# Optimization experiments

Hardware: AMD Instinct MI355X
Metric: run time of the kernel (lower is better)

The kernel has to match this reference:

```python
import jax, jax.numpy as jnp
import numpy as np

DIM = 768
NUM_HEADS = 12
HEAD_DIM = DIM // NUM_HEADS
SCALE = HEAD_DIM ** -0.5


def setup_inputs() -> dict:
    key = jax.random.key(0)
    ks = jax.random.split(key, 6)
    B, Lq, Lkv = 8, 1024, 1024
    return {
        "q": jax.random.normal(ks[0], (B, Lq, DIM), dtype=jnp.float32),
        "kv": jax.random.normal(ks[1], (B, Lkv, DIM), dtype=jnp.float32),
        "attn_pos": jax.random.normal(ks[2], (1, NUM_HEADS, Lq, Lkv), dtype=jnp.float32),
        "Wq": jax.random.normal(ks[3], (DIM, DIM), dtype=jnp.float32) * (DIM ** -0.5),
        "Wkv": jax.random.normal(ks[4], (2 * DIM, DIM), dtype=jnp.float32) * (DIM ** -0.5),
        "Wproj": jax.random.normal(ks[5], (DIM, DIM), dtype=jnp.float32) * (DIM ** -0.5),
        "bproj": jnp.zeros((DIM,), dtype=jnp.float32),
    }


def reference(q, kv, attn_pos, Wq, Wkv, Wproj, bproj):
    B, Lq, C = q.shape
    Lkv = kv.shape[1]
    H, D = NUM_HEADS, HEAD_DIM
    # q/kv projections (torch Linear: x @ W.T); attn_pos_encoding_only path
    qh = (q @ Wq.T).reshape(B, Lq, H, D).transpose(0, 2, 1, 3)        # (B,H,Lq,D)
    kvp = (kv @ Wkv.T).reshape(B, Lkv, 2, H, D).transpose(2, 0, 3, 1, 4)
    k, v = kvp[0], kvp[1]                                             # (B,H,Lkv,D)
    # scaled dot-product attention with additive positional bias
    attn = jnp.einsum('bhqd,bhkd->bhqk', qh, k) * SCALE + attn_pos    # (B,H,Lq,Lkv)
    attn = jax.nn.softmax(attn, axis=-1)
    x = jnp.einsum('bhqk,bhkd->bhqd', attn, v)                        # (B,H,Lq,D)
    x = x.transpose(0, 2, 1, 3).reshape(B, Lq, C)
    return x @ Wproj.T + bproj
```

## Files before the change

kernel.cpp:

```cpp
#include <hip/hip_runtime.h>

#define DIM 768
#define NHEADS 12
#define HDIM 64
#define BATCH 8
#define LQ 1024
#define LKV 1024
#define ATTN_SCALE 0.125f
#define LOG2E 1.4426950408889634f
#define C1_SL2E 0.18033688011112042f

typedef __bf16 bf16;
typedef __bf16 bf16x4 __attribute__((ext_vector_type(4)));
typedef __bf16 bf16x8 __attribute__((ext_vector_type(8)));
typedef short s16x4 __attribute__((ext_vector_type(4)));
typedef float f32x4 __attribute__((ext_vector_type(4)));

union B4 { bf16x4 h; s16x4 s; };

static __device__ __forceinline__ f32x4 mfma_k32(bf16x8 a, bf16x8 b, f32x4 c) {
    return __builtin_amdgcn_mfma_f32_16x16x32_bf16(a, b, c, 0, 0, 0);
}
static __device__ __forceinline__ f32x4 mfma_k16(s16x4 a, s16x4 b, f32x4 c) {
    return __builtin_amdgcn_mfma_f32_16x16x16bf16_1k(a, b, c, 0, 0, 0);
}

static __device__ __forceinline__ void async16(const bf16* g, bf16* l) {
    __builtin_amdgcn_global_load_lds(
        (const __attribute__((address_space(1))) unsigned int*)g,
        (__attribute__((address_space(3))) unsigned int*)l, 16, 0, 0);
}
static __device__ __forceinline__ void drain_vmem() {
    __asm__ volatile("s_waitcnt vmcnt(0)" ::: "memory");
}
#define WAIT_VMCNT(N) __asm__ volatile("s_waitcnt vmcnt(" #N ")" ::: "memory")
static __device__ __forceinline__ void code_fence() {
    __asm__ volatile("" ::: "memory");
}

#define NQ4 (BATCH * LQ * DIM / 4)
#define NW4 (DIM * DIM / 4)
__global__ void cvt_all(const float4* __restrict__ q, const float4* __restrict__ kv,
                        const float4* __restrict__ Wq, const float4* __restrict__ Wkv,
                        const float4* __restrict__ Wp,
                        bf16x4* __restrict__ qb, bf16x4* __restrict__ kvb,
                        bf16x4* __restrict__ wall, bf16x4* __restrict__ wpb) {
    int i = blockIdx.x * 256 + threadIdx.x;
    const float4* src; bf16x4* dst; int j;
    if (i < NQ4)                { src = q;   dst = qb;        j = i; }
    else if (i < 2 * NQ4)       { src = kv;  dst = kvb;       j = i - NQ4; }
    else if (i < 2 * NQ4 + NW4) { src = Wq;  dst = wall;      j = i - 2 * NQ4; }
    else if (i < 2 * NQ4 + 3 * NW4) { src = Wkv; dst = wall + NW4; j = i - 2 * NQ4 - NW4; }
    else if (i < 2 * NQ4 + 4 * NW4) { src = Wp;  dst = wpb;   j = i - 2 * NQ4 - 3 * NW4; }
    else return;
    float4 v = src[j];
    bf16x4 o;
    o[0] = (bf16)v.x; o[1] = (bf16)v.y; o[2] = (bf16)v.z; o[3] = (bf16)v.w;
    dst[j] = o;
}

__global__ __launch_bounds__(256) void proj_gemm(
    const bf16* __restrict__ qb, const bf16* __restrict__ kvb,
    const bf16* __restrict__ W,
    bf16* __restrict__ Qp, bf16* __restrict__ Kp, bf16* __restrict__ Vt)
{
    __shared__ bf16 As[2][128 * 32];
    __shared__ bf16 Bs[2][128 * 32];
    const int tid  = threadIdx.x;
    const int lane = tid & 63;
    const int w    = tid >> 6;
    const int wm = (w >> 1) * 64;
    const int wn = (w & 1) * 64;
    const int m0 = blockIdx.x * 128;
    const int n0 = blockIdx.y * 128;
    const int K = DIM;
    const int lq = lane & 15;
    const int quad = lane >> 4;

    const bf16* A = (n0 < DIM) ? qb : kvb;
    const int isV = (n0 >= 2 * DIM);

    const int rl = lane >> 2;
    const int ck = (lane & 3) * 8;
    const bf16* gA = A + (size_t)(m0 + w * 32 + rl) * K + ck;
    const bf16* gB = W + (size_t)(n0 + w * 32 + rl) * K + ck;

    f32x4 acc[4][4] = {};

#define PSTAGE(K0, BUFI) do {                                          \
    async16(gA + (K0),                  &As[BUFI][w * 1024]);          \
    async16(gA + (size_t)16 * K + (K0), &As[BUFI][w * 1024 + 512]);    \
    async16(gB + (K0),                  &Bs[BUFI][w * 1024]);          \
    async16(gB + (size_t)16 * K + (K0), &Bs[BUFI][w * 1024 + 512]);    \
} while (0)

    PSTAGE(0, 0);
    drain_vmem();
    __syncthreads();

    for (int k0 = 0; k0 < K; k0 += 32) {
        const int cur = (k0 >> 5) & 1;
        const bool more = (k0 + 32 < K);
        if (more) PSTAGE(k0 + 32, cur ^ 1);

        bf16x8 a[4], b[4];
        #pragma unroll
        for (int i = 0; i < 4; i++)
            a[i] = *(const bf16x8*)&As[cur][(wm + i * 16 + lq) * 32 + quad * 8];
        #pragma unroll
        for (int j = 0; j < 4; j++)
            b[j] = *(const bf16x8*)&Bs[cur][(wn + j * 16 + lq) * 32 + quad * 8];
        if (isV) {
            #pragma unroll
            for (int i = 0; i < 4; i++)
                #pragma unroll
                for (int j = 0; j < 4; j++)
                    acc[i][j] = mfma_k32(a[i], b[j], acc[i][j]);
        } else {
            #pragma unroll
            for (int i = 0; i < 4; i++)
                #pragma unroll
                for (int j = 0; j < 4; j++)
                    acc[i][j] = mfma_k32(b[j], a[i], acc[i][j]);
        }

        if (more) drain_vmem();
        __syncthreads();
    }
#undef PSTAGE

    if (isV) {
        const int n0v = n0 - 2 * DIM;
        #pragma unroll
        for (int i = 0; i < 4; i++) {
            const int base_m = m0 + wm + i * 16;
            const int b_idx = base_m >> 10;
            const int kvl = (base_m & 1023) + quad * 4;
            #pragma unroll
            for (int j = 0; j < 4; j++) {
                const int nl = n0v + wn + j * 16 + lq;
                const int h = nl >> 6;
                const int d = nl & 63;
                B4 pk;
                #pragma unroll
                for (int r = 0; r < 4; r++) pk.h[r] = (bf16)acc[i][j][r];
                *(s16x4*)&Vt[(((size_t)b_idx * NHEADS + h) * HDIM + d) * LKV + kvl] = pk.s;
            }
        }
    } else {
        bf16* Cb = (n0 < DIM) ? Qp : Kp;
        const float cs = (n0 < DIM) ? C1_SL2E : 1.0f;
        const int nb = (n0 < DIM) ? n0 : n0 - DIM;
        #pragma unroll
        for (int i = 0; i < 4; i++) {
            const size_t row = m0 + wm + i * 16 + lq;
            #pragma unroll
            for (int j = 0; j < 4; j++) {
                const int col = nb + wn + j * 16 + quad * 4;
                B4 pk;
                #pragma unroll
                for (int r = 0; r < 4; r++) pk.h[r] = (bf16)(acc[i][j][r] * cs);
                *(s16x4*)&Cb[row * DIM + col] = pk.s;
            }
        }
    }
}

__global__ __launch_bounds__(256) void out_gemm(
    const bf16* __restrict__ A, const bf16* __restrict__ B,
    float* __restrict__ Cp, const float* __restrict__ bias, int M, int N, int K)
{
    __shared__ bf16 As[2][64 * 32];
    __shared__ bf16 Bs[2][128 * 32];
    const int tid  = threadIdx.x;
    const int lane = tid & 63;
    const int w    = tid >> 6;
    const int wm = (w >> 1) * 32;
    const int wn = (w & 1) * 64;
    const int m0 = blockIdx.x * 64;
    const int n0 = blockIdx.y * 128;
    const int lq = lane & 15;
    const int quad = lane >> 4;

    const int rl = lane >> 2;
    const int ck = (lane & 3) * 8;
    const bf16* gA = A + (size_t)(m0 + w * 16 + rl) * K + ck;
    const bf16* gB = B + (size_t)(n0 + w * 32 + rl) * K + ck;

    f32x4 acc[2][4] = {};

#define OSTAGE(K0, BUFI) do {                                          \
    async16(gA + (K0),                  &As[BUFI][w * 512]);           \
    async16(gB + (K0),                  &Bs[BUFI][w * 1024]);          \
    async16(gB + (size_t)16 * K + (K0), &Bs[BUFI][w * 1024 + 512]);    \
} while (0)

    OSTAGE(0, 0);
    drain_vmem();
    __syncthreads();

    for (int k0 = 0; k0 < K; k0 += 32) {
        const int cur = (k0 >> 5) & 1;
        const bool more = (k0 + 32 < K);
        if (more) OSTAGE(k0 + 32, cur ^ 1);

        bf16x8 a[2], b[4];
        #pragma unroll
        for (int i = 0; i < 2; i++)
            a[i] = *(const bf16x8*)&As[cur][(wm + i * 16 + lq) * 32 + quad * 8];
        #pragma unroll
        for (int j = 0; j < 4; j++)
            b[j] = *(const bf16x8*)&Bs[cur][(wn + j * 16 + lq) * 32 + quad * 8];
        #pragma unroll
        for (int i = 0; i < 2; i++)
            #pragma unroll
            for (int j = 0; j < 4; j++)
                acc[i][j] = mfma_k32(b[j], a[i], acc[i][j]);

        if (more) drain_vmem();
        __syncthreads();
    }
#undef OSTAGE

    #pragma unroll
    for (int i = 0; i < 2; i++) {
        const size_t row = m0 + wm + i * 16 + lq;
        #pragma unroll
        for (int j = 0; j < 4; j++) {
            const int col = n0 + wn + j * 16 + quad * 4;
            float4 bj = *(const float4*)&bias[col];
            float4 o;
            o.x = acc[i][j][0] + bj.x; o.y = acc[i][j][1] + bj.y;
            o.z = acc[i][j][2] + bj.z; o.w = acc[i][j][3] + bj.w;
            *(float4*)&Cp[row * N + col] = o;
        }
    }
}

__global__ __launch_bounds__(256) void attn_kernel(
    const bf16* __restrict__ Qb,
    const bf16* __restrict__ Kb,
    const bf16* __restrict__ Vt,
    const float* __restrict__ pos,
    bf16* __restrict__ O)
{
    __shared__ bf16 Ks[2][64 * 64];
    __shared__ bf16 Vs[2][64 * 64];

    const int by = blockIdx.y;
    const int h = by >> 3, b = by & 7;
    const int bh = b * NHEADS + h;
    const int q0 = blockIdx.x * 64;
    const int t = threadIdx.x;
    const int lane = t & 63;
    const int w = t >> 6;
    const int lq = lane & 15;
    const int quad = lane >> 4;

    const bf16* qg = Qb + (size_t)(b * LQ + q0 + w * 16 + lq) * DIM + h * HDIM + quad * 8;
    bf16x8 qa0 = *(const bf16x8*)(qg);
    bf16x8 qa1 = *(const bf16x8*)(qg + 32);

    const int srow  = t >> 3;
    const int chunk = t & 7;
    const int sw    = (chunk ^ (srow & 7)) * 8;
    const bf16* Kg = Kb + (size_t)(b * LKV + srow) * DIM + h * HDIM + sw;
    const bf16* Vg = Vt + (size_t)(bh * HDIM + srow) * LKV + sw;

#define STAGE(kv0, bufi) do {                                                                 \
    async16(Kg + (size_t)(kv0) * DIM,        &Ks[bufi][srow * 64 + chunk * 8]);               \
    async16(Kg + (size_t)((kv0) + 32) * DIM, &Ks[bufi][(srow + 32) * 64 + chunk * 8]);        \
    async16(Vg + (kv0),                      &Vs[bufi][srow * 64 + chunk * 8]);               \
    async16(Vg + (size_t)32 * LKV + (kv0),   &Vs[bufi][(srow + 32) * 64 + chunk * 8]);        \
} while (0)

#define NT (LKV / 64)

    const float4* pos4 = (const float4*)(pos + ((size_t)h * LQ + q0 + w * 16 + lq) * LKV);

    float l_r = 0.f;
    f32x4 o_acc[4] = {};

    STAGE(0, 0);
    float4 pA0 = pos4[quad],      pA1 = pos4[4 + quad];
    float4 pA2 = pos4[8 + quad],  pA3 = pos4[12 + quad];
    float4 pB0 = pos4[16 + quad], pB1 = pos4[20 + quad];
    float4 pB2 = pos4[24 + quad], pB3 = pos4[28 + quad];
    WAIT_VMCNT(8);
    __builtin_amdgcn_s_barrier();
    code_fence();

#define SMB(KB, P) do {                                          \
    float p0 = exp2f(fmaf((P).x, LOG2E, sc[KB][0]));             \
    float p1 = exp2f(fmaf((P).y, LOG2E, sc[KB][1]));             \
    float p2 = exp2f(fmaf((P).z, LOG2E, sc[KB][2]));             \
    float p3 = exp2f(fmaf((P).w, LOG2E, sc[KB][3]));             \
    l_r += (p0 + p1) + (p2 + p3);                                \
    pfrag[KB].h[0] = (bf16)p0; pfrag[KB].h[1] = (bf16)p1;        \
    pfrag[KB].h[2] = (bf16)p2; pfrag[KB].h[3] = (bf16)p3;        \
} while (0)

#define BODY(IT, BUF, P0, P1, P2, P3) do {                                                     \
    if ((IT) + 1 < NT) STAGE(((IT) + 1) * 64, (BUF) ^ 1);                                      \
    f32x4 sc[4];                                                                               \
    __builtin_amdgcn_s_setprio(1);                                                             \
    _Pragma("unroll")                                                                          \
    for (int kb = 0; kb < 4; kb++) {                                                           \
        const int krow = kb * 16 + lq;                                                         \
        bf16x8 ak0 = *(const bf16x8*)&Ks[BUF][krow * 64 + ((quad) ^ (lq & 7)) * 8];            \
        bf16x8 ak1 = *(const bf16x8*)&Ks[BUF][krow * 64 + ((4 + quad) ^ (lq & 7)) * 8];        \
        sc[kb] = mfma_k32(ak0, qa0, (f32x4){0.f, 0.f, 0.f, 0.f});                              \
        sc[kb] = mfma_k32(ak1, qa1, sc[kb]);                                                   \
    }                                                                                          \
    __builtin_amdgcn_s_setprio(0);                                                             \
    B4 pfrag[4];                                                                               \
    SMB(0, P0); SMB(1, P1); SMB(2, P2); SMB(3, P3);                                            \
    if ((IT) + 2 < NT) {                                                                       \
        const int pb = ((IT) + 2) * 16 + quad;                                                 \
        P0 = pos4[pb]; P1 = pos4[pb + 4]; P2 = pos4[pb + 8]; P3 = pos4[pb + 12];               \
    }                                                                                          \
    __builtin_amdgcn_s_setprio(1);                                                             \
    _Pragma("unroll")                                                                          \
    for (int db = 0; db < 4; db++) {                                                           \
        const int vrow = db * 16 + lq;                                                         \
        _Pragma("unroll")                                                                      \
        for (int kb = 0; kb < 4; kb++) {                                                       \
            s16x4 va = *(const s16x4*)&Vs[BUF][vrow * 64                                       \
                          + (((kb * 2 + (quad >> 1)) ^ (lq & 7)) * 8) + (quad & 1) * 4];       \
            o_acc[db] = mfma_k16(va, pfrag[kb].s, o_acc[db]);                                  \
        }                                                                                      \
    }                                                                                          \
    __builtin_amdgcn_s_setprio(0);                                                             \
    if ((IT) + 1 < NT) {                                                                       \
        WAIT_VMCNT(4);                             \
        __builtin_amdgcn_s_barrier();                           \
        code_fence();                                  \
    }                                                                                          \
} while (0)

    for (int it2 = 0; it2 < NT; it2 += 2) {
        BODY(it2,     0, pA0, pA1, pA2, pA3);
        BODY(it2 + 1, 1, pB0, pB1, pB2, pB3);
    }
#undef BODY
#undef SMB
#undef STAGE

    l_r += __shfl_xor(l_r, 16);
    l_r += __shfl_xor(l_r, 32);
    float inv = 1.f / l_r;
    const size_t orow = (size_t)(b * LQ + q0 + w * 16 + lq) * DIM + h * HDIM;
    #pragma unroll
    for (int dblk = 0; dblk < 4; dblk++) {
        B4 ob;
        #pragma unroll
        for (int r = 0; r < 4; r++) ob.h[r] = (bf16)(o_acc[dblk][r] * inv);
        *(s16x4*)&O[orow + dblk * 16 + quad * 4] = ob.s;
    }
}

extern "C" void kernel_launch(void* const* d_in, const int* in_sizes, int n_in,
                              void* d_out, int out_size, void* d_ws, size_t ws_size,
                              hipStream_t stream) {
    const float* q     = (const float*)d_in[0];
    const float* kv    = (const float*)d_in[1];
    const float* pos   = (const float*)d_in[2];
    const float* Wq    = (const float*)d_in[3];
    const float* Wkv   = (const float*)d_in[4];
    const float* Wproj = (const float*)d_in[5];
    const float* bproj = (const float*)d_in[6];
    float* out = (float*)d_out;

    char* ws = (char*)d_ws;
    size_t off = 0;
    auto alloc = [&](size_t bytes) -> void* {
        void* p = ws + off;
        off += (bytes + 255) & ~(size_t)255;
        return p;
    };

    const int M = BATCH * LQ;
    bf16* qb   = (bf16*)alloc((size_t)M * DIM * 2);
    bf16* kvb  = (bf16*)alloc((size_t)M * DIM * 2);
    bf16* wall = (bf16*)alloc((size_t)3 * DIM * DIM * 2);
    bf16* wpb  = (bf16*)alloc((size_t)DIM * DIM * 2);
    bf16* Qp   = (bf16*)alloc((size_t)M * DIM * 2);
    bf16* Kp   = (bf16*)alloc((size_t)M * DIM * 2);
    bf16* Vt   = (bf16*)alloc((size_t)BATCH * NHEADS * HDIM * LKV * 2);
    bf16* Ob   = (bf16*)alloc((size_t)M * DIM * 2);

    {
        int total = 2 * NQ4 + 4 * NW4;
        cvt_all<<<(total + 255) / 256, 256, 0, stream>>>(
            (const float4*)q, (const float4*)kv, (const float4*)Wq,
            (const float4*)Wkv, (const float4*)Wproj,
            (bf16x4*)qb, (bf16x4*)kvb, (bf16x4*)wall, (bf16x4*)wpb);
    }

    proj_gemm<<<dim3(M / 128, (3 * DIM) / 128), 256, 0, stream>>>(qb, kvb, wall, Qp, Kp, Vt);
    attn_kernel<<<dim3(LQ / 64, NHEADS * BATCH), 256, 0, stream>>>(Qp, Kp, Vt, pos, Ob);
    out_gemm<<<dim3(M / 64, DIM / 128), 256, 0, stream>>>(Ob, wpb, out, bproj, M, DIM, DIM);
}
```

Before: 297.1 us.

## Remap attention grid for XCD-local pos reuse and single-buffer GEMM tiles

The attention launch becomes a 1D grid with a swizzled index. Blocks on the same XCD (i&7) now cover the same head and query tiles across all batches, so the batch-shared attn_pos bias and related data can be reused from that XCD's L2. Separately, both projection GEMMs drop double-buffered LDS staging in favour of a single buffer: load, drain, sync, compute, sync. That reduces LDS use and may raise occupancy, but it gives up overlap between global loads and MFMA work.

```diff
diff --git a/kernel.cpp b/kernel.cpp
--- a/kernel.cpp
+++ b/kernel.cpp
@@ -64,8 +64,8 @@
     const bf16* __restrict__ W,
     bf16* __restrict__ Qp, bf16* __restrict__ Kp, bf16* __restrict__ Vt)
 {
-    __shared__ bf16 As[2][128 * 32];
-    __shared__ bf16 Bs[2][128 * 32];
+    __shared__ bf16 As[128 * 32];
+    __shared__ bf16 Bs[128 * 32];
     const int tid  = threadIdx.x;
     const int lane = tid & 63;
     const int w    = tid >> 6;
@@ -84,32 +84,26 @@
     const int ck = (lane & 3) * 8;
     const bf16* gA = A + (size_t)(m0 + w * 32 + rl) * K + ck;
     const bf16* gB = W + (size_t)(n0 + w * 32 + rl) * K + ck;
+    bf16* lA = &As[w * 1024];
+    bf16* lB = &Bs[w * 1024];
 
     f32x4 acc[4][4] = {};
 
-#define PSTAGE(K0, BUFI) do {                                          \
-    async16(gA + (K0),                  &As[BUFI][w * 1024]);          \
-    async16(gA + (size_t)16 * K + (K0), &As[BUFI][w * 1024 + 512]);    \
-    async16(gB + (K0),                  &Bs[BUFI][w * 1024]);          \
-    async16(gB + (size_t)16 * K + (K0), &Bs[BUFI][w * 1024 + 512]);    \
-} while (0)
-
-    PSTAGE(0, 0);
-    drain_vmem();
-    __syncthreads();
-
     for (int k0 = 0; k0 < K; k0 += 32) {
-        const int cur = (k0 >> 5) & 1;
-        const bool more = (k0 + 32 < K);
-        if (more) PSTAGE(k0 + 32, cur ^ 1);
+        async16(gA + k0,                  lA);
+        async16(gA + (size_t)16 * K + k0, lA + 512);
+        async16(gB + k0,                  lB);
+        async16(gB + (size_t)16 * K + k0, lB + 512);
+        drain_vmem();
+        __syncthreads();
 
         bf16x8 a[4], b[4];
         #pragma unroll
         for (int i = 0; i < 4; i++)
-            a[i] = *(const bf16x8*)&As[cur][(wm + i * 16 + lq) * 32 + quad * 8];
+            a[i] = *(const bf16x8*)&As[(wm + i * 16 + lq) * 32 + quad * 8];
         #pragma unroll
         for (int j = 0; j < 4; j++)
-            b[j] = *(const bf16x8*)&Bs[cur][(wn + j * 16 + lq) * 32 + quad * 8];
+            b[j] = *(const bf16x8*)&Bs[(wn + j * 16 + lq) * 32 + quad * 8];
         if (isV) {
             #pragma unroll
             for (int i = 0; i < 4; i++)
@@ -123,11 +117,8 @@
                 for (int j = 0; j < 4; j++)
                     acc[i][j] = mfma_k32(b[j], a[i], acc[i][j]);
         }
-
-        if (more) drain_vmem();
         __syncthreads();
     }
-#undef PSTAGE
 
     if (isV) {
         const int n0v = n0 - 2 * DIM;
@@ -170,8 +161,8 @@
     const bf16* __restrict__ A, const bf16* __restrict__ B,
     float* __restrict__ Cp, const float* __restrict__ bias, int M, int N, int K)
 {
-    __shared__ bf16 As[2][64 * 32];
-    __shared__ bf16 Bs[2][128 * 32];
+    __shared__ bf16 As[64 * 32];
+    __shared__ bf16 Bs[128 * 32];
     const int tid  = threadIdx.x;
     const int lane = tid & 63;
     const int w    = tid >> 6;
@@ -186,41 +177,32 @@
     const int ck = (lane & 3) * 8;
     const bf16* gA = A + (size_t)(m0 + w * 16 + rl) * K + ck;
     const bf16* gB = B + (size_t)(n0 + w * 32 + rl) * K + ck;
+    bf16* lA = &As[w * 512];
+    bf16* lB = &Bs[w * 1024];
 
     f32x4 acc[2][4] = {};
 
-#define OSTAGE(K0, BUFI) do {                                          \
-    async16(gA + (K0),                  &As[BUFI][w * 512]);           \
-    async16(gB + (K0),                  &Bs[BUFI][w * 1024]);          \
-    async16(gB + (size_t)16 * K + (K0), &Bs[BUFI][w * 1024 + 512]);    \
-} while (0)
-
-    OSTAGE(0, 0);
-    drain_vmem();
-    __syncthreads();
-
     for (int k0 = 0; k0 < K; k0 += 32) {
-        const int cur = (k0 >> 5) & 1;
-        const bool more = (k0 + 32 < K);
-        if (more) OSTAGE(k0 + 32, cur ^ 1);
+        async16(gA + k0,                  lA);
+        async16(gB + k0,                  lB);
+        async16(gB + (size_t)16 * K + k0, lB + 512);
+        drain_vmem();
+        __syncthreads();
 
         bf16x8 a[2], b[4];
         #pragma unroll
         for (int i = 0; i < 2; i++)
-            a[i] = *(const bf16x8*)&As[cur][(wm + i * 16 + lq) * 32 + quad * 8];
+            a[i] = *(const bf16x8*)&As[(wm + i * 16 + lq) * 32 + quad * 8];
         #pragma unroll
         for (int j = 0; j < 4; j++)
-            b[j] = *(const bf16x8*)&Bs[cur][(wn + j * 16 + lq) * 32 + quad * 8];
+            b[j] = *(const bf16x8*)&Bs[(wn + j * 16 + lq) * 32 + quad * 8];
         #pragma unroll
         for (int i = 0; i < 2; i++)
             #pragma unroll
             for (int j = 0; j < 4; j++)
                 acc[i][j] = mfma_k32(b[j], a[i], acc[i][j]);
-
-        if (more) drain_vmem();
         __syncthreads();
     }
-#undef OSTAGE
 
     #pragma unroll
     for (int i = 0; i < 2; i++) {
@@ -247,10 +229,12 @@
     __shared__ bf16 Ks[2][64 * 64];
     __shared__ bf16 Vs[2][64 * 64];
 
-    const int by = blockIdx.y;
-    const int h = by >> 3, b = by & 7;
+    const int i  = blockIdx.x;
+    const int g  = (i & 7) * 24 + (i >> 6);
+    const int b  = (i >> 3) & 7;
+    const int h  = g >> 4;
+    const int q0 = (g & 15) * 64;
     const int bh = b * NHEADS + h;
-    const int q0 = blockIdx.x * 64;
     const int t = threadIdx.x;
     const int lane = t & 63;
     const int w = t >> 6;
@@ -398,6 +382,6 @@
     }
 
     proj_gemm<<<dim3(M / 128, (3 * DIM) / 128), 256, 0, stream>>>(qb, kvb, wall, Qp, Kp, Vt);
-    attn_kernel<<<dim3(LQ / 64, NHEADS * BATCH), 256, 0, stream>>>(Qp, Kp, Vt, pos, Ob);
+    attn_kernel<<<dim3((LQ / 64) * NHEADS * BATCH), 256, 0, stream>>>(Qp, Kp, Vt, pos, Ob);
     out_gemm<<<dim3(M / 64, DIM / 128), 256, 0, stream>>>(Ob, wpb, out, bproj, M, DIM, DIM);
 }
```

Result: faster. 285.3 us (-4.0%).
